# Optimization experiments

Hardware: AMD Instinct MI355X
Metric: run time of the kernel (lower is better)

## Reference

```python
import jax, jax.numpy as jnp
import numpy as np

B, V, T, S, C, NH, H, MULT = 1, 2, 2, 16384, 128, 9, 4, 2
DH = C // H


def _ln(x, g, b):
    m = jnp.mean(x, -1, keepdims=True)
    v = jnp.mean((x - m) ** 2, -1, keepdims=True)
    return (x - m) * jax.lax.rsqrt(v + 1e-5) * g + b


def setup_inputs():
    key = jax.random.key(0)
    ks = jax.random.split(key, 16)
    sc = 0.02
    return {
        "x": jax.random.normal(ks[0], (B, V, T, S, C), jnp.float32),
        "adjc": jax.random.randint(ks[1], (S, NH), 0, S, dtype=jnp.int32),
        "mask": jax.random.bernoulli(ks[2], 0.1, (B, V, T, S)),
        "ln1_g": jnp.ones((C,), jnp.float32),
        "ln1_b": jnp.zeros((C,), jnp.float32),
        "Wq": sc * jax.random.normal(ks[3], (C, C), jnp.float32),
        "Wkv": sc * jax.random.normal(ks[4], (C, 2 * C), jnp.float32),
        "b_kv": jnp.zeros((2 * C,), jnp.float32),
        "W_nh": sc * jax.random.normal(ks[5], (NH, NH), jnp.float32),
        "W_ao": sc * jax.random.normal(ks[6], (C, C), jnp.float32),
        "ln2_g": jnp.ones((C,), jnp.float32),
        "ln2_b": jnp.zeros((C,), jnp.float32),
        "W1": sc * jax.random.normal(ks[7], (C, MULT * C), jnp.float32),
        "b1": jnp.zeros((MULT * C,), jnp.float32),
        "W2": sc * jax.random.normal(ks[8], (MULT * C, C), jnp.float32),
        "b2": jnp.zeros((C,), jnp.float32),
        "gamma": 0.1 * jnp.ones((C,), jnp.float32),
        "Wout": sc * jax.random.normal(ks[9], (C, C), jnp.float32),
    }


def reference(x, adjc, mask, ln1_g, ln1_b, Wq, Wkv, b_kv, W_nh, W_ao,
              ln2_g, ln2_b, W1, b1, W2, b2, gamma, Wout):
    # 1. per-zoom embedding layer (LayerNorm, identity linear)
    xe = _ln(x, ln1_g, ln1_b)  # [b,v,t,s,c]
    # 2. query projection, q_len = 1 per grid cell
    q = jnp.einsum("bvtsc,cd->bvtsd", xe, Wq)
    # 3. neighborhood gather (grid_layer.get_nh) + fused KV projection
    kv_nh = xe[:, :, :, adjc, :]                       # [b,v,t,s,nh,c]
    kv = jnp.einsum("bvtsnc,cd->bvtsnd", kv_nh, Wkv) + b_kv  # [b,v,t,s,nh,2c]
    # factorized nh-mixing with residual skip (skip_dims=[True,...])
    kv = kv + jnp.einsum("bvtsnd,nm->bvtsmd", kv, W_nh)
    # 4. gathered neighbor mask (True = masked out)
    m_nh = mask[:, :, :, adjc]                          # [b,v,t,s,nh]
    # 5. multi-head cross attention, q_len=1, kv_len=nh
    k, v = jnp.split(kv, 2, axis=-1)                    # each [b,v,t,s,nh,c]
    qh = q.reshape(B, V, T, S, H, DH)
    kh = k.reshape(B, V, T, S, NH, H, DH)
    vh = v.reshape(B, V, T, S, NH, H, DH)
    scores = jnp.einsum("bvtshd,bvtsnhd->bvtshn", qh, kh) / jnp.sqrt(
        jnp.asarray(DH, qh.dtype))
    scores = jnp.where(m_nh[:, :, :, :, None, :], -1e9, scores)
    attn = jax.nn.softmax(scores, axis=-1)
    o = jnp.einsum("bvtshn,bvtsnhd->bvtshd", attn, vh).reshape(B, V, T, S, C)
    o = jnp.einsum("bvtsc,cd->bvtsd", o, W_ao)
    # 6. residual insert
    x = x + o
    # 7. MLP block with layer-scale gamma
    xm = _ln(x, ln2_g, ln2_b)
    h = jax.nn.gelu(jnp.einsum("bvtsc,cd->bvtsd", xm, W1) + b1)
    x = x + gamma * (jnp.einsum("bvtsd,dc->bvtsc", h, W2) + b2)
    # 8. output layer
    return jnp.einsum("bvtsc,cd->bvtsd", x, Wout)
```

## Files before the change

kernel.cpp:

```cpp
#include <hip/hip_runtime.h>
#include <math.h>

namespace {

typedef float f32x4 __attribute__((ext_vector_type(4)));
typedef short s16x8 __attribute__((ext_vector_type(8)));

constexpr int C_   = 128;
constexpr int S_   = 16384;
constexpr int NTOK = 65536;

__device__ __forceinline__ unsigned short f2bf(float f) {
    unsigned int u = __float_as_uint(f);
    unsigned int r = (u + 0x7FFFu + ((u >> 16) & 1u)) >> 16;
    return (unsigned short)r;
}
__device__ __forceinline__ float bf2f(unsigned short h) {
    return __uint_as_float(((unsigned int)h) << 16);
}
__device__ __forceinline__ float gelu_tanh(float v) {
    const float k0 = 0.7978845608028654f;
    float u = k0 * (v + 0.044715f * v * v * v);
    float au = fabsf(u);
    float E = __expf(2.0f * au);
    float th = 1.0f - 2.0f / (1.0f + E);
    th = (u < 0.f) ? -th : th;
    return 0.5f * v * (1.0f + th);
}

__global__ __launch_bounds__(256) void prep_weights(
    const float* __restrict__ Wq, const float* __restrict__ Wkv,
    const float* __restrict__ W_ao, const float* __restrict__ W1,
    const float* __restrict__ W2, const float* __restrict__ Wout,
    unsigned short* __restrict__ Wf)
{
    int idx = blockIdx.x * 256 + threadIdx.x;
    if (idx >= 147456) return;
    int seg, off, K, N; const float* src = nullptr;
    if (idx < 49152)       { seg = 0; off = 0;      K = 128; N = 384; }
    else if (idx < 65536)  { seg = 1; off = 49152;  K = 128; N = 128; src = W_ao; }
    else if (idx < 98304)  { seg = 2; off = 65536;  K = 128; N = 256; src = W1; }
    else if (idx < 131072) { seg = 3; off = 98304;  K = 256; N = 128; src = W2; }
    else                   { seg = 4; off = 131072; K = 128; N = 128; src = Wout; }
    int local = idx - off;
    int j    = local & 7;
    int lane = (local >> 3) & 63;
    int tl   = local >> 9;
    int KB   = K >> 5;
    int kb   = tl % KB;
    int nt   = tl / KB;
    int k    = kb * 32 + ((lane >> 4) << 3) + j;
    int col  = (nt << 4) + (lane & 15);
    float v;
    if (seg == 0) v = (col < 128) ? Wq[k * 128 + col] : Wkv[k * 256 + (col - 128)];
    else          v = src[k * N + col];
    Wf[idx] = f2bf(v);
}

__global__ __launch_bounds__(256, 2) void qkv_kernel(
    const float* __restrict__ x,
    const float* __restrict__ ln1_g, const float* __restrict__ ln1_b,
    const unsigned short* __restrict__ Wf,
    const float* __restrict__ b_kv,
    float* qout, unsigned short* __restrict__ kout,
    unsigned short* __restrict__ vout)
{
    __shared__ unsigned short xet[32 * 128];
    const int tile = blockIdx.x;
    const int t = threadIdx.x;

    {
        const int row = t >> 3;
        const int j   = t & 7;
        const int tok = tile * 32 + row;
        const float* xr = x + (size_t)tok * C_ + j * 16;
        float v[16];
        float s0 = 0.f, s1 = 0.f;
        #pragma unroll
        for (int i = 0; i < 16; i += 4) {
            float4 f = *(const float4*)(xr + i);
            v[i] = f.x; v[i+1] = f.y; v[i+2] = f.z; v[i+3] = f.w;
            s0 += f.x + f.y + f.z + f.w;
            s1 += f.x*f.x + f.y*f.y + f.z*f.z + f.w*f.w;
        }
        s0 += __shfl_xor(s0, 1, 64); s1 += __shfl_xor(s1, 1, 64);
        s0 += __shfl_xor(s0, 2, 64); s1 += __shfl_xor(s1, 2, 64);
        s0 += __shfl_xor(s0, 4, 64); s1 += __shfl_xor(s1, 4, 64);
        const float mean = s0 * (1.0f / C_);
        const float var  = s1 * (1.0f / C_) - mean * mean;
        const float inv  = rsqrtf(var + 1e-5f);
        unsigned short tmp[16];
        #pragma unroll
        for (int i = 0; i < 16; ++i) {
            int c = j * 16 + i;
            tmp[i] = f2bf((v[i] - mean) * inv * ln1_g[c] + ln1_b[c]);
        }
        int b0 = (row * 256 + j * 32) ^ ((row & 7) << 4);
        int b1_ = (row * 256 + j * 32 + 16) ^ ((row & 7) << 4);
        *(s16x8*)((char*)xet + b0)  = *(const s16x8*)tmp;
        *(s16x8*)((char*)xet + b1_) = *(const s16x8*)(tmp + 8);
    }
    __syncthreads();

    const int w = t >> 6, l = t & 63;
    const int wr = w >> 1, wc = w & 1;
    const int arow = (wr << 4) + (l & 15);
    s16x8 af[4];
    #pragma unroll
    for (int kb = 0; kb < 4; ++kb) {
        int byte = arow * 256 + (kb * 32 + ((l >> 4) << 3)) * 2;
        byte ^= (arow & 7) << 4;
        af[kb] = *(const s16x8*)((const char*)xet + byte);
    }
    f32x4 acc[12];
    #pragma unroll
    for (int nt = 0; nt < 12; ++nt) acc[nt] = (f32x4){0.f, 0.f, 0.f, 0.f};
    #pragma unroll
    for (int nt = 0; nt < 12; ++nt) {
        const int ntg = wc * 12 + nt;
        #pragma unroll
        for (int kb = 0; kb < 4; ++kb) {
            s16x8 bf = *(const s16x8*)(Wf + (size_t)((ntg * 4 + kb) * 64 + l) * 8);
            acc[nt] = __builtin_amdgcn_mfma_f32_16x16x32_bf16(af[kb], bf, acc[nt], 0, 0, 0);
        }
    }
    const int crow0 = (wr << 4) + ((l >> 4) << 2);
    const int colb = l & 15;
    #pragma unroll
    for (int nt = 0; nt < 12; ++nt) {
        const int gcol = (wc * 12 + nt) * 16 + colb;
        #pragma unroll
        for (int reg = 0; reg < 4; ++reg) {
            const size_t tokr = (size_t)tile * 32 + crow0 + reg;
            const float val = acc[nt][reg];
            if (gcol < 128) {
                qout[tokr * 128 + gcol] = val;
            } else if (gcol < 256) {
                const int ch = gcol - 128;
                kout[tokr * 128 + ch] = f2bf(val + b_kv[ch]);
            } else {
                const int ch = gcol - 256;
                vout[tokr * 128 + ch] = f2bf(val + b_kv[ch + 128]);
            }
        }
    }
}

__global__ __launch_bounds__(256, 2) void attn_mlp_kernel(
    const float* __restrict__ x,
    const int* __restrict__ adjc, const unsigned char* __restrict__ mask,
    const float* __restrict__ wnh,
    const float* __restrict__ qbuf,
    const unsigned short* __restrict__ kbuf,
    const unsigned short* __restrict__ vbuf,
    const unsigned short* __restrict__ Wao_f, const unsigned short* __restrict__ W1f,
    const unsigned short* __restrict__ W2f, const unsigned short* __restrict__ Woutf,
    const float* __restrict__ ln2_g, const float* __restrict__ ln2_b,
    const float* __restrict__ b1, const float* __restrict__ b2,
    const float* __restrict__ gamma,
    float* outp)
{
    __shared__ unsigned short act[8192];
    __shared__ float sred[2][32][2];
    __shared__ unsigned int sidx[32][9];

    const int d   = blockIdx.x;
    const int xcd = d & 7, dj = d >> 3;
    const int bid = (xcd >> 1) * 512 + dj * 2 + (xcd & 1);
    const size_t base = (size_t)bid * 32;
    const int s0  = (int)(base & (S_ - 1));
    const int bvt = (int)(base >> 14);
    const int t = threadIdx.x;

    for (int i = t; i < 288; i += 256) {
        int r = i / 9, n = i - r * 9;
        int nb = adjc[(s0 + r) * 9 + n];
        unsigned int gi = (unsigned int)(bvt * S_ + nb);
        sidx[r][n] = gi | (mask[gi] ? 0x80000000u : 0u);
    }
    __syncthreads();

    {
        const int r = t >> 3, j = t & 7;
        const size_t tok = base + r;

        float q[16];
        {
            const float4* qp = (const float4*)(qbuf + tok * 128 + j * 16);
            #pragma unroll
            for (int i = 0; i < 4; ++i) {
                float4 f = qp[i];
                q[4*i] = f.x; q[4*i+1] = f.y; q[4*i+2] = f.z; q[4*i+3] = f.w;
            }
        }
        unsigned int gm[9];
        #pragma unroll
        for (int n = 0; n < 9; ++n) gm[n] = sidx[r][n];

        float sp[9];
        #pragma unroll
        for (int n = 0; n < 9; ++n) {
            const s16x8* kp = (const s16x8*)(kbuf +
                (size_t)(gm[n] & 0x7fffffffu) * 128 + j * 16);
            s16x8 k0 = kp[0], k1 = kp[1];
            float a = 0.f;
            #pragma unroll
            for (int i = 0; i < 8; ++i) a += q[i]     * bf2f((unsigned short)k0[i]);
            #pragma unroll
            for (int i = 0; i < 8; ++i) a += q[8 + i] * bf2f((unsigned short)k1[i]);
            sp[n] = a;
        }
        #pragma unroll
        for (int n = 0; n < 9; ++n) sp[n] += __shfl_xor(sp[n], 1, 64);

        float S[9];
        #pragma unroll
        for (int m = 0; m < 9; ++m) {
            float a = sp[m];
            #pragma unroll
            for (int n = 0; n < 9; ++n) a += sp[n] * wnh[n * 9 + m];
            a *= 0.17677669529663687f;
            S[m] = (gm[m] & 0x80000000u) ? -1e9f : a;
        }
        float mx = S[0];
        #pragma unroll
        for (int m = 1; m < 9; ++m) mx = fmaxf(mx, S[m]);
        float e[9], se = 0.f;
        #pragma unroll
        for (int m = 0; m < 9; ++m) { e[m] = __expf(S[m] - mx); se += e[m]; }
        const float inv = 1.f / se;

        float ap[9];
        #pragma unroll
        for (int n = 0; n < 9; ++n) {
            float a = e[n];
            #pragma unroll
            for (int m = 0; m < 9; ++m) a += wnh[n * 9 + m] * e[m];
            ap[n] = a * inv;
        }

        float o[16];
        #pragma unroll
        for (int i = 0; i < 16; ++i) o[i] = 0.f;
        #pragma unroll
        for (int n = 0; n < 9; ++n) {
            const s16x8* vp = (const s16x8*)(vbuf +
                (size_t)(gm[n] & 0x7fffffffu) * 128 + j * 16);
            s16x8 v0 = vp[0], v1 = vp[1];
            const float a = ap[n];
            #pragma unroll
            for (int i = 0; i < 8; ++i) o[i]     += a * bf2f((unsigned short)v0[i]);
            #pragma unroll
            for (int i = 0; i < 8; ++i) o[8 + i] += a * bf2f((unsigned short)v1[i]);
        }
        unsigned short tmp[16];
        #pragma unroll
        for (int i = 0; i < 16; ++i) tmp[i] = f2bf(o[i]);
        int b0 = (r * 256 + j * 32) ^ ((r & 7) << 4);
        int b1_ = (r * 256 + j * 32 + 16) ^ ((r & 7) << 4);
        *(s16x8*)((char*)act + b0)  = *(const s16x8*)tmp;
        *(s16x8*)((char*)act + b1_) = *(const s16x8*)(tmp + 8);
    }
    __syncthreads();

    const int w = t >> 6, l = t & 63;
    const int wr = w >> 1, wc = w & 1;
    const int arow = (wr << 4) + (l & 15);
    const int crow0 = (wr << 4) + ((l >> 4) << 2);
    const int colb = l & 15;

    s16x8 af[4];
    #pragma unroll
    for (int kb = 0; kb < 4; ++kb) {
        int byte = arow * 256 + (kb * 32 + ((l >> 4) << 3)) * 2;
        byte ^= (arow & 7) << 4;
        af[kb] = *(const s16x8*)((const char*)act + byte);
    }
    f32x4 acc1[4];
    #pragma unroll
    for (int nt = 0; nt < 4; ++nt) acc1[nt] = (f32x4){0.f, 0.f, 0.f, 0.f};
    #pragma unroll
    for (int nt = 0; nt < 4; ++nt) {
        const int ntg = wc * 4 + nt;
        #pragma unroll
        for (int kb = 0; kb < 4; ++kb) {
            s16x8 bf = *(const s16x8*)(Wao_f + (size_t)((ntg * 4 + kb) * 64 + l) * 8);
            acc1[nt] = __builtin_amdgcn_mfma_f32_16x16x32_bf16(af[kb], bf, acc1[nt], 0, 0, 0);
        }
    }

    float x1v[4][4];
    float ss[4] = {0.f, 0.f, 0.f, 0.f}, s2[4] = {0.f, 0.f, 0.f, 0.f};
    #pragma unroll
    for (int nt = 0; nt < 4; ++nt) {
        const int col = wc * 64 + nt * 16 + colb;
        #pragma unroll
        for (int reg = 0; reg < 4; ++reg) {
            const size_t tokr = base + crow0 + reg;
            float xv = x[tokr * 128 + col] + acc1[nt][reg];
            x1v[nt][reg] = xv;
            ss[reg] += xv;
            s2[reg] += xv * xv;
        }
    }
    #pragma unroll
    for (int off = 1; off < 16; off <<= 1) {
        #pragma unroll
        for (int reg = 0; reg < 4; ++reg) {
            ss[reg] += __shfl_xor(ss[reg], off, 64);
            s2[reg] += __shfl_xor(s2[reg], off, 64);
        }
    }
    if (colb == 0) {
        #pragma unroll
        for (int reg = 0; reg < 4; ++reg) {
            sred[wc][crow0 + reg][0] = ss[reg];
            sred[wc][crow0 + reg][1] = s2[reg];
        }
    }
    __syncthreads();
    float mean[4], inv[4];
    #pragma unroll
    for (int reg = 0; reg < 4; ++reg) {
        const int row = crow0 + reg;
        float sum = sred[0][row][0] + sred[1][row][0];
        float sq  = sred[0][row][1] + sred[1][row][1];
        mean[reg] = sum * (1.0f / 128.f);
        float var = sq * (1.0f / 128.f) - mean[reg] * mean[reg];
        inv[reg] = rsqrtf(var + 1e-5f);
    }
    __syncthreads();
    #pragma unroll
    for (int nt = 0; nt < 4; ++nt) {
        const int col = wc * 64 + nt * 16 + colb;
        const float lg = ln2_g[col], lb = ln2_b[col];
        #pragma unroll
        for (int reg = 0; reg < 4; ++reg) {
            const int lrow = crow0 + reg;
            float xm = (x1v[nt][reg] - mean[reg]) * inv[reg] * lg + lb;
            int byte = lrow * 256 + col * 2;
            byte ^= (lrow & 7) << 4;
            *(unsigned short*)((char*)act + byte) = f2bf(xm);
        }
    }
    __syncthreads();

    #pragma unroll
    for (int kb = 0; kb < 4; ++kb) {
        int byte = arow * 256 + (kb * 32 + ((l >> 4) << 3)) * 2;
        byte ^= (arow & 7) << 4;
        af[kb] = *(const s16x8*)((const char*)act + byte);
    }
    f32x4 acc2[8];
    #pragma unroll
    for (int nt = 0; nt < 8; ++nt) acc2[nt] = (f32x4){0.f, 0.f, 0.f, 0.f};
    #pragma unroll
    for (int nt = 0; nt < 8; ++nt) {
        const int ntg = wc * 8 + nt;
        #pragma unroll
        for (int kb = 0; kb < 4; ++kb) {
            s16x8 bf = *(const s16x8*)(W1f + (size_t)((ntg * 4 + kb) * 64 + l) * 8);
            acc2[nt] = __builtin_amdgcn_mfma_f32_16x16x32_bf16(af[kb], bf, acc2[nt], 0, 0, 0);
        }
    }
    __syncthreads();
    #pragma unroll
    for (int nt = 0; nt < 8; ++nt) {
        const int col2 = wc * 128 + nt * 16 + colb;
        const float bb = b1[col2];
        #pragma unroll
        for (int reg = 0; reg < 4; ++reg) {
            const int lrow = crow0 + reg;
            float hv = gelu_tanh(acc2[nt][reg] + bb);
            int byte = lrow * 512 + col2 * 2;
            byte ^= (lrow & 7) << 4;
            *(unsigned short*)((char*)act + byte) = f2bf(hv);
        }
    }
    __syncthreads();

    f32x4 acc3[4];
    #pragma unroll
    for (int nt = 0; nt < 4; ++nt) acc3[nt] = (f32x4){0.f, 0.f, 0.f, 0.f};
    #pragma unroll
    for (int kb = 0; kb < 8; ++kb) {
        int byte = arow * 512 + (kb * 32 + ((l >> 4) << 3)) * 2;
        byte ^= (arow & 7) << 4;
        s16x8 hf = *(const s16x8*)((const char*)act + byte);
        #pragma unroll
        for (int nt = 0; nt < 4; ++nt) {
            const int ntg = wc * 4 + nt;
            s16x8 bf = *(const s16x8*)(W2f + (size_t)((ntg * 8 + kb) * 64 + l) * 8);
            acc3[nt] = __builtin_amdgcn_mfma_f32_16x16x32_bf16(hf, bf, acc3[nt], 0, 0, 0);
        }
    }
    __syncthreads();
    #pragma unroll
    for (int nt = 0; nt < 4; ++nt) {
        const int col = wc * 64 + nt * 16 + colb;
        const float gm = gamma[col], bb = b2[col];
        #pragma unroll
        for (int reg = 0; reg < 4; ++reg) {
            const int lrow = crow0 + reg;
            float y = x1v[nt][reg] + gm * (acc3[nt][reg] + bb);
            int byte = lrow * 256 + col * 2;
            byte ^= (lrow & 7) << 4;
            *(unsigned short*)((char*)act + byte) = f2bf(y);
        }
    }
    __syncthreads();

    #pragma unroll
    for (int kb = 0; kb < 4; ++kb) {
        int byte = arow * 256 + (kb * 32 + ((l >> 4) << 3)) * 2;
        byte ^= (arow & 7) << 4;
        af[kb] = *(const s16x8*)((const char*)act + byte);
    }
    f32x4 acc4[4];
    #pragma unroll
    for (int nt = 0; nt < 4; ++nt) acc4[nt] = (f32x4){0.f, 0.f, 0.f, 0.f};
    #pragma unroll
    for (int nt = 0; nt < 4; ++nt) {
        const int ntg = wc * 4 + nt;
        #pragma unroll
        for (int kb = 0; kb < 4; ++kb) {
            s16x8 bf = *(const s16x8*)(Woutf + (size_t)((ntg * 4 + kb) * 64 + l) * 8);
            acc4[nt] = __builtin_amdgcn_mfma_f32_16x16x32_bf16(af[kb], bf, acc4[nt], 0, 0, 0);
        }
    }
    #pragma unroll
    for (int nt = 0; nt < 4; ++nt) {
        const int col = wc * 64 + nt * 16 + colb;
        #pragma unroll
        for (int reg = 0; reg < 4; ++reg) {
            const size_t tokr = base + crow0 + reg;
            outp[tokr * 128 + col] = acc4[nt][reg];
        }
    }
}

}

extern "C" void kernel_launch(void* const* d_in, const int* in_sizes, int n_in,
                              void* d_out, int out_size, void* d_ws, size_t ws_size,
                              hipStream_t stream) {
    const float* x     = (const float*)d_in[0];
    const int*   adjc  = (const int*)d_in[1];
    const unsigned char* mask = (const unsigned char*)d_in[2];
    const float* ln1_g = (const float*)d_in[3];
    const float* ln1_b = (const float*)d_in[4];
    const float* Wq    = (const float*)d_in[5];
    const float* Wkv   = (const float*)d_in[6];
    const float* b_kv  = (const float*)d_in[7];
    const float* W_nh  = (const float*)d_in[8];
    const float* W_ao  = (const float*)d_in[9];
    const float* ln2_g = (const float*)d_in[10];
    const float* ln2_b = (const float*)d_in[11];
    const float* W1    = (const float*)d_in[12];
    const float* b1    = (const float*)d_in[13];
    const float* W2    = (const float*)d_in[14];
    const float* b2    = (const float*)d_in[15];
    const float* gamma = (const float*)d_in[16];
    const float* Wout  = (const float*)d_in[17];

    unsigned short* kbuf = (unsigned short*)d_ws;
    unsigned short* vbuf = kbuf + (size_t)NTOK * 128;
    unsigned short* Wf   = vbuf + (size_t)NTOK * 128;
    unsigned short* Wao_f  = Wf + 49152;
    unsigned short* W1f    = Wf + 65536;
    unsigned short* W2f    = Wf + 98304;
    unsigned short* Woutf  = Wf + 131072;

    float* qbuf = (float*)d_out;

    prep_weights<<<576, 256, 0, stream>>>(Wq, Wkv, W_ao, W1, W2, Wout, Wf);
    qkv_kernel<<<NTOK / 32, 256, 0, stream>>>(x, ln1_g, ln1_b, Wf, b_kv,
                                              qbuf, kbuf, vbuf);
    attn_mlp_kernel<<<NTOK / 32, 256, 0, stream>>>(x, adjc, mask, W_nh,
                                                   qbuf, kbuf, vbuf,
                                                   Wao_f, W1f, W2f, Woutf,
                                                   ln2_g, ln2_b, b1, b2, gamma,
                                                   (float*)d_out);
}
```

Measured before the change: 135.5 us.

## Shrink token tiles to 16 rows with 128-thread blocks and inline neighbor index gather

Both the QKV and the fused attention/MLP kernels now process 16 tokens per block with two waves instead of 32 tokens with four waves. Each wave covers the full 16-row strip and half of the output columns, so the block grid doubles and launch bounds ask for more resident blocks per CU. The shared-memory neighbor index table and its barrier are removed; each thread reads adjc and mask directly into registers. The aim is more blocks in flight to hide gather and global-memory latency. In exchange, each block reuses the B-fragment weight loads over fewer rows, and threads sharing a token load the same adjacency entries redundantly.

```diff
diff --git a/kernel.cpp b/kernel.cpp
--- a/kernel.cpp
+++ b/kernel.cpp
@@ -57,7 +57,7 @@
     Wf[idx] = f2bf(v);
 }
 
-__global__ __launch_bounds__(256, 2) void qkv_kernel(
+__global__ __launch_bounds__(128, 4) void qkv_kernel(
     const float* __restrict__ x,
     const float* __restrict__ ln1_g, const float* __restrict__ ln1_b,
     const unsigned short* __restrict__ Wf,
@@ -65,14 +65,14 @@
     float* qout, unsigned short* __restrict__ kout,
     unsigned short* __restrict__ vout)
 {
-    __shared__ unsigned short xet[32 * 128];
+    __shared__ unsigned short xet[16 * 128];
     const int tile = blockIdx.x;
     const int t = threadIdx.x;
 
     {
         const int row = t >> 3;
         const int j   = t & 7;
-        const int tok = tile * 32 + row;
+        const int tok = tile * 16 + row;
         const float* xr = x + (size_t)tok * C_ + j * 16;
         float v[16];
         float s0 = 0.f, s1 = 0.f;
@@ -103,8 +103,7 @@
     __syncthreads();
 
     const int w = t >> 6, l = t & 63;
-    const int wr = w >> 1, wc = w & 1;
-    const int arow = (wr << 4) + (l & 15);
+    const int arow = l & 15;
     s16x8 af[4];
     #pragma unroll
     for (int kb = 0; kb < 4; ++kb) {
@@ -117,21 +116,21 @@
     for (int nt = 0; nt < 12; ++nt) acc[nt] = (f32x4){0.f, 0.f, 0.f, 0.f};
     #pragma unroll
     for (int nt = 0; nt < 12; ++nt) {
-        const int ntg = wc * 12 + nt;
+        const int ntg = w * 12 + nt;
         #pragma unroll
         for (int kb = 0; kb < 4; ++kb) {
             s16x8 bf = *(const s16x8*)(Wf + (size_t)((ntg * 4 + kb) * 64 + l) * 8);
             acc[nt] = __builtin_amdgcn_mfma_f32_16x16x32_bf16(af[kb], bf, acc[nt], 0, 0, 0);
         }
     }
-    const int crow0 = (wr << 4) + ((l >> 4) << 2);
+    const int crow0 = (l >> 4) << 2;
     const int colb = l & 15;
     #pragma unroll
     for (int nt = 0; nt < 12; ++nt) {
-        const int gcol = (wc * 12 + nt) * 16 + colb;
-        #pragma unroll
-        for (int reg = 0; reg < 4; ++reg) {
-            const size_t tokr = (size_t)tile * 32 + crow0 + reg;
+        const int gcol = (w * 12 + nt) * 16 + colb;
+        #pragma unroll
+        for (int reg = 0; reg < 4; ++reg) {
+            const size_t tokr = (size_t)tile * 16 + crow0 + reg;
             const float val = acc[nt][reg];
             if (gcol < 128) {
                 qout[tokr * 128 + gcol] = val;
@@ -146,7 +145,7 @@
     }
 }
 
-__global__ __launch_bounds__(256, 2) void attn_mlp_kernel(
+__global__ __launch_bounds__(128, 6) void attn_mlp_kernel(
     const float* __restrict__ x,
     const int* __restrict__ adjc, const unsigned char* __restrict__ mask,
     const float* __restrict__ wnh,
@@ -160,30 +159,30 @@
     const float* __restrict__ gamma,
     float* outp)
 {
-    __shared__ unsigned short act[8192];
-    __shared__ float sred[2][32][2];
-    __shared__ unsigned int sidx[32][9];
+    __shared__ unsigned short act[4096];
+    __shared__ float sred[2][16][2];
 
     const int d   = blockIdx.x;
     const int xcd = d & 7, dj = d >> 3;
-    const int bid = (xcd >> 1) * 512 + dj * 2 + (xcd & 1);
-    const size_t base = (size_t)bid * 32;
+    const int bid = (xcd >> 1) * 1024 + dj * 2 + (xcd & 1);
+    const size_t base = (size_t)bid * 16;
     const int s0  = (int)(base & (S_ - 1));
     const int bvt = (int)(base >> 14);
     const int t = threadIdx.x;
 
-    for (int i = t; i < 288; i += 256) {
-        int r = i / 9, n = i - r * 9;
-        int nb = adjc[(s0 + r) * 9 + n];
-        unsigned int gi = (unsigned int)(bvt * S_ + nb);
-        sidx[r][n] = gi | (mask[gi] ? 0x80000000u : 0u);
-    }
-    __syncthreads();
-
     {
         const int r = t >> 3, j = t & 7;
         const size_t tok = base + r;
 
+        unsigned int gm[9];
+        {
+            const int* ar = adjc + (s0 + r) * 9;
+            #pragma unroll
+            for (int n = 0; n < 9; ++n) {
+                unsigned int gi = (unsigned int)(bvt * S_ + ar[n]);
+                gm[n] = gi | (mask[gi] ? 0x80000000u : 0u);
+            }
+        }
         float q[16];
         {
             const float4* qp = (const float4*)(qbuf + tok * 128 + j * 16);
@@ -193,9 +192,6 @@
                 q[4*i] = f.x; q[4*i+1] = f.y; q[4*i+2] = f.z; q[4*i+3] = f.w;
             }
         }
-        unsigned int gm[9];
-        #pragma unroll
-        for (int n = 0; n < 9; ++n) gm[n] = sidx[r][n];
 
         float sp[9];
         #pragma unroll
@@ -264,9 +260,8 @@
     __syncthreads();
 
     const int w = t >> 6, l = t & 63;
-    const int wr = w >> 1, wc = w & 1;
-    const int arow = (wr << 4) + (l & 15);
-    const int crow0 = (wr << 4) + ((l >> 4) << 2);
+    const int arow = l & 15;
+    const int crow0 = (l >> 4) << 2;
     const int colb = l & 15;
 
     s16x8 af[4];
@@ -281,7 +276,7 @@
     for (int nt = 0; nt < 4; ++nt) acc1[nt] = (f32x4){0.f, 0.f, 0.f, 0.f};
     #pragma unroll
     for (int nt = 0; nt < 4; ++nt) {
-        const int ntg = wc * 4 + nt;
+        const int ntg = w * 4 + nt;
         #pragma unroll
         for (int kb = 0; kb < 4; ++kb) {
             s16x8 bf = *(const s16x8*)(Wao_f + (size_t)((ntg * 4 + kb) * 64 + l) * 8);
@@ -293,7 +288,7 @@
     float ss[4] = {0.f, 0.f, 0.f, 0.f}, s2[4] = {0.f, 0.f, 0.f, 0.f};
     #pragma unroll
     for (int nt = 0; nt < 4; ++nt) {
-        const int col = wc * 64 + nt * 16 + colb;
+        const int col = w * 64 + nt * 16 + colb;
         #pragma unroll
         for (int reg = 0; reg < 4; ++reg) {
             const size_t tokr = base + crow0 + reg;
@@ -314,8 +309,8 @@
     if (colb == 0) {
         #pragma unroll
         for (int reg = 0; reg < 4; ++reg) {
-            sred[wc][crow0 + reg][0] = ss[reg];
-            sred[wc][crow0 + reg][1] = s2[reg];
+            sred[w][crow0 + reg][0] = ss[reg];
+            sred[w][crow0 + reg][1] = s2[reg];
         }
     }
     __syncthreads();
@@ -332,7 +327,7 @@
     __syncthreads();
     #pragma unroll
     for (int nt = 0; nt < 4; ++nt) {
-        const int col = wc * 64 + nt * 16 + colb;
+        const int col = w * 64 + nt * 16 + colb;
         const float lg = ln2_g[col], lb = ln2_b[col];
         #pragma unroll
         for (int reg = 0; reg < 4; ++reg) {
@@ -356,7 +351,7 @@
     for (int nt = 0; nt < 8; ++nt) acc2[nt] = (f32x4){0.f, 0.f, 0.f, 0.f};
     #pragma unroll
     for (int nt = 0; nt < 8; ++nt) {
-        const int ntg = wc * 8 + nt;
+        const int ntg = w * 8 + nt;
         #pragma unroll
         for (int kb = 0; kb < 4; ++kb) {
             s16x8 bf = *(const s16x8*)(W1f + (size_t)((ntg * 4 + kb) * 64 + l) * 8);
@@ -366,7 +361,7 @@
     __syncthreads();
     #pragma unroll
     for (int nt = 0; nt < 8; ++nt) {
-        const int col2 = wc * 128 + nt * 16 + colb;
+        const int col2 = w * 128 + nt * 16 + colb;
         const float bb = b1[col2];
         #pragma unroll
         for (int reg = 0; reg < 4; ++reg) {
@@ -389,7 +384,7 @@
         s16x8 hf = *(const s16x8*)((const char*)act + byte);
         #pragma unroll
         for (int nt = 0; nt < 4; ++nt) {
-            const int ntg = wc * 4 + nt;
+            const int ntg = w * 4 + nt;
             s16x8 bf = *(const s16x8*)(W2f + (size_t)((ntg * 8 + kb) * 64 + l) * 8);
             acc3[nt] = __builtin_amdgcn_mfma_f32_16x16x32_bf16(hf, bf, acc3[nt], 0, 0, 0);
         }
@@ -397,7 +392,7 @@
     __syncthreads();
     #pragma unroll
     for (int nt = 0; nt < 4; ++nt) {
-        const int col = wc * 64 + nt * 16 + colb;
+        const int col = w * 64 + nt * 16 + colb;
         const float gm = gamma[col], bb = b2[col];
         #pragma unroll
         for (int reg = 0; reg < 4; ++reg) {
@@ -421,7 +416,7 @@
     for (int nt = 0; nt < 4; ++nt) acc4[nt] = (f32x4){0.f, 0.f, 0.f, 0.f};
     #pragma unroll
     for (int nt = 0; nt < 4; ++nt) {
-        const int ntg = wc * 4 + nt;
+        const int ntg = w * 4 + nt;
         #pragma unroll
         for (int kb = 0; kb < 4; ++kb) {
             s16x8 bf = *(const s16x8*)(Woutf + (size_t)((ntg * 4 + kb) * 64 + l) * 8);
@@ -430,7 +425,7 @@
     }
     #pragma unroll
     for (int nt = 0; nt < 4; ++nt) {
-        const int col = wc * 64 + nt * 16 + colb;
+        const int col = w * 64 + nt * 16 + colb;
         #pragma unroll
         for (int reg = 0; reg < 4; ++reg) {
             const size_t tokr = base + crow0 + reg;
@@ -474,9 +469,9 @@
     float* qbuf = (float*)d_out;
 
     prep_weights<<<576, 256, 0, stream>>>(Wq, Wkv, W_ao, W1, W2, Wout, Wf);
-    qkv_kernel<<<NTOK / 32, 256, 0, stream>>>(x, ln1_g, ln1_b, Wf, b_kv,
+    qkv_kernel<<<NTOK / 16, 128, 0, stream>>>(x, ln1_g, ln1_b, Wf, b_kv,
                                               qbuf, kbuf, vbuf);
-    attn_mlp_kernel<<<NTOK / 32, 256, 0, stream>>>(x, adjc, mask, W_nh,
+    attn_mlp_kernel<<<NTOK / 16, 128, 0, stream>>>(x, adjc, mask, W_nh,
                                                    qbuf, kbuf, vbuf,
                                                    Wao_f, W1f, W2f, Woutf,
                                                    ln2_g, ln2_b, b1, b2, gamma,
```

After: 214.7 us. 58.4% more time.
